# Kernel optimization log

Measured on AMD Instinct MI355X. Metric: run time of the kernel, lower is better.

## Reference

```python
import jax, jax.numpy as jnp
import numpy as np

VOCAB, NUM_TAGS, EMB, HID = 30000, 20, 200, 128
B, S = 128, 512


def setup_inputs() -> dict:
    key = jax.random.key(0)
    ks = jax.random.split(key, 13)
    sentence = jax.random.randint(ks[0], (B, S), 0, VOCAB)
    tags = jax.random.randint(ks[1], (B, S), 0, NUM_TAGS)
    lengths = jax.random.randint(ks[2], (B,), 1, S + 1)
    mask = jnp.arange(S)[None, :] < lengths[:, None]  # [B,S] bool, mask[:,0] all True
    sc = 0.1
    return {
        "sentence": sentence,
        "tags": tags,
        "mask": mask,
        "embedding": jax.random.normal(ks[3], (VOCAB, EMB), jnp.float32) * sc,
        "W_ih": jax.random.normal(ks[4], (4 * HID, EMB), jnp.float32) * sc,
        "W_hh": jax.random.normal(ks[5], (4 * HID, HID), jnp.float32) * sc,
        "b_ih": jax.random.normal(ks[6], (4 * HID,), jnp.float32) * sc,
        "b_hh": jax.random.normal(ks[7], (4 * HID,), jnp.float32) * sc,
        "W_dec": jax.random.normal(ks[8], (NUM_TAGS, HID), jnp.float32) * sc,
        "b_dec": jax.random.normal(ks[9], (NUM_TAGS,), jnp.float32) * sc,
        "start_trans": jax.random.normal(ks[10], (NUM_TAGS,), jnp.float32) * sc,
        "end_trans": jax.random.normal(ks[11], (NUM_TAGS,), jnp.float32) * sc,
        "trans": jax.random.normal(ks[12], (NUM_TAGS, NUM_TAGS), jnp.float32) * sc,
    }


def _lstm(embeds, W_ih, W_hh, b_ih, b_hh):
    # torch nn.LSTM, single layer, batch_first, zero init state; gate order i,f,g,o
    b = embeds.shape[0]
    h0 = jnp.zeros((b, HID), embeds.dtype)
    x = jnp.swapaxes(embeds, 0, 1)  # [S,B,E]
    xg = jnp.einsum('sbe,ge->sbg', x, W_ih) + b_ih + b_hh  # input projections, [S,B,4H]

    def step(carry, xg_t):
        h, c = carry
        g = xg_t + h @ W_hh.T
        i, f, gg, o = jnp.split(g, 4, axis=-1)
        c = jax.nn.sigmoid(f) * c + jax.nn.sigmoid(i) * jnp.tanh(gg)
        h = jax.nn.sigmoid(o) * jnp.tanh(c)
        return (h, c), h

    _, hs = jax.lax.scan(step, (h0, h0), xg)
    return jnp.swapaxes(hs, 0, 1)  # [B,S,H]


def _crf_nll_mean(emissions, tags, mask, start_trans, end_trans, trans):
    # torchcrf.CRF negative log likelihood, reduction='mean' (mean over batch)
    b = emissions.shape[0]
    ems = jnp.swapaxes(emissions, 0, 1)          # [S,B,T]
    tgs = jnp.swapaxes(tags, 0, 1)               # [S,B]
    msk = jnp.swapaxes(mask, 0, 1).astype(emissions.dtype)  # [S,B]
    bidx = jnp.arange(b)

    # numerator: score of the gold path
    num0 = start_trans[tgs[0]] + ems[0, bidx, tgs[0]]

    def nstep(score, inp):
        em, tag, ptag, m = inp
        return score + (trans[ptag, tag] + em[bidx, tag]) * m, None

    num, _ = jax.lax.scan(nstep, num0, (ems[1:], tgs[1:], tgs[:-1], msk[1:]))
    last_idx = mask.sum(axis=1).astype(jnp.int32) - 1
    num = num + end_trans[tags[bidx, last_idx]]

    # denominator: forward algorithm (log partition)
    sc0 = start_trans[None, :] + ems[0]  # [B,T]

    def dstep(score, inp):
        em, m = inp
        nxt = jax.nn.logsumexp(score[:, :, None] + trans[None] + em[:, None, :], axis=1)
        return jnp.where(m[:, None] > 0, nxt, score), None

    sc, _ = jax.lax.scan(dstep, sc0, (ems[1:], msk[1:]))
    den = jax.nn.logsumexp(sc + end_trans[None, :], axis=1)
    return -jnp.mean(num - den)


def reference(sentence, tags, mask, embedding, W_ih, W_hh, b_ih, b_hh,
              W_dec, b_dec, start_trans, end_trans, trans):
    embeds = embedding[sentence]                           # [B,S,E]
    lstm_out = _lstm(embeds, W_ih, W_hh, b_ih, b_hh)       # [B,S,H]
    emissions = jnp.einsum('bsh,th->bst', lstm_out, W_dec) + b_dec  # [B,S,T]
    # dropout treated as identity (eval-mode reference)
    return _crf_nll_mean(emissions, tags, mask, start_trans, end_trans, trans)
```

## Files before the change

### kernel.cpp

```cpp
#include <hip/hip_runtime.h>
#include <hip/hip_bf16.h>
#include <hip/hip_fp16.h>
#include <math.h>

#define B_ 128
#define S_ 512
#define EMB_ 200
#define HID_ 128
#define NT_ 20
#define G4_ 512
#define KP_ 224

typedef _Float16 f16x2_t __attribute__((ext_vector_type(2)));
typedef short bf16x8 __attribute__((ext_vector_type(8)));
typedef float f32x4 __attribute__((ext_vector_type(4)));

#if __has_builtin(__builtin_amdgcn_fdot2)
#define FDOT2(a, b, c) __builtin_amdgcn_fdot2(__builtin_bit_cast(f16x2_t, (a)), \
                                              __builtin_bit_cast(f16x2_t, (b)), (c), false)
#else
static __device__ __forceinline__ float fdot2_fb(unsigned a, unsigned b, float c) {
    float alo = __half2float(__ushort_as_half((unsigned short)(a & 0xffffu)));
    float ahi = __half2float(__ushort_as_half((unsigned short)(a >> 16)));
    float blo = __half2float(__ushort_as_half((unsigned short)(b & 0xffffu)));
    float bhi = __half2float(__ushort_as_half((unsigned short)(b >> 16)));
    return c + alo * blo + ahi * bhi;
}
#define FDOT2(a, b, c) fdot2_fb((a), (b), (c))
#endif

__device__ __forceinline__ float bf2f(unsigned u) {
    union { unsigned u; float f; } cv;
    cv.u = u << 16;
    return cv.f;
}
__device__ __forceinline__ unsigned packh2(float a, float b) {
    return ((unsigned)__half_as_ushort(__float2half(b)) << 16)
         | (unsigned)__half_as_ushort(__float2half(a));
}
__device__ __forceinline__ unsigned short f2bf(float f) {
    __hip_bfloat16 h = __float2bfloat16(f);
    unsigned short u;
    __builtin_memcpy(&u, &h, 2);
    return u;
}

__global__ void k_detect(const unsigned char* mask, int* flag) {
    __shared__ int partial[4];
    int tid = threadIdx.x;
    int s = 0;
    for (int i = tid; i < B_ * S_; i += 256) {
        if (i & 3) s += mask[i];
    }
    for (int m = 32; m >= 1; m >>= 1) s += __shfl_xor(s, m);
    if ((tid & 63) == 0) partial[tid >> 6] = s;
    __syncthreads();
    if (tid == 0) {
        int tot = partial[0] + partial[1] + partial[2] + partial[3];
        flag[0] = (tot > 0) ? 1 : 0;
    }
}

__global__ void k_prep(const float* __restrict__ W_ih, const float* __restrict__ b_ih,
                       const float* __restrict__ b_hh, __hip_bfloat16* __restrict__ Wb,
                       float* __restrict__ biasb) {
    int i = blockIdx.x * 256 + threadIdx.x;
    if (i < G4_ * KP_) {
        int g = i / KP_, k = i - g * KP_;
        float v = (k < EMB_) ? W_ih[g * EMB_ + k] : 0.f;
        Wb[i] = __float2bfloat16(v);
    }
    if (i < G4_) biasb[i] = b_ih[i] + b_hh[i];
}

__global__ __launch_bounds__(256, 2) void k_xg(const int* __restrict__ sentence,
                                               const float* __restrict__ embedding,
                                               const __hip_bfloat16* __restrict__ Wb,
                                               const float* __restrict__ biasb,
                                               __hip_bfloat16* __restrict__ xg) {
    __shared__ short Bl[G4_ * 40];
    __shared__ short Al[32 * 40];
    __shared__ int ids_s[32];
    int tid = threadIdx.x;
    int m0 = blockIdx.x * 32;
    int lane = tid & 63;
    int gbase = (tid >> 6) * 128;
    if (tid < 32) ids_s[tid] = sentence[m0 + tid];
    __syncthreads();

    f32x4 acc0[8], acc1[8];
#pragma unroll
    for (int n = 0; n < 8; n++) {
        acc0[n] = (f32x4){0.f, 0.f, 0.f, 0.f};
        acc1[n] = (f32x4){0.f, 0.f, 0.f, 0.f};
    }
    int lrow = lane & 15, lk = lane >> 4;

    for (int c = 0; c < 7; c++) {
        int k0 = c * 32;
#pragma unroll
        for (int i = 0; i < 8; i++) {
            int idx = tid + 256 * i;
            int row = idx >> 2, q = idx & 3;
            uint4 v = *(const uint4*)((const short*)Wb + (size_t)row * KP_ + k0 + q * 8);
            *(uint4*)(Bl + row * 40 + q * 8) = v;
        }
#pragma unroll
        for (int i = 0; i < 2; i++) {
            int j = tid + 256 * i;
            int row = j >> 4, kp = j & 15;
            int k = k0 + kp * 2;
            const float* e = embedding + (size_t)ids_s[row] * EMB_;
            float v0 = (k < EMB_) ? e[k] : 0.f;
            float v1 = (k + 1 < EMB_) ? e[k + 1] : 0.f;
            unsigned u = (unsigned)f2bf(v0) | ((unsigned)f2bf(v1) << 16);
            *(unsigned*)(Al + row * 40 + kp * 2) = u;
        }
        __syncthreads();
        bf16x8 a0 = *(const bf16x8*)(Al + lrow * 40 + lk * 8);
        bf16x8 a1 = *(const bf16x8*)(Al + (lrow + 16) * 40 + lk * 8);
#pragma unroll
        for (int n = 0; n < 8; n++) {
            bf16x8 bfr = *(const bf16x8*)(Bl + (gbase + n * 16 + lrow) * 40 + lk * 8);
            acc0[n] = __builtin_amdgcn_mfma_f32_16x16x32_bf16(a0, bfr, acc0[n], 0, 0, 0);
            acc1[n] = __builtin_amdgcn_mfma_f32_16x16x32_bf16(a1, bfr, acc1[n], 0, 0, 0);
        }
        __syncthreads();
    }
    int rbase = m0 + lk * 4;
#pragma unroll
    for (int n = 0; n < 8; n++) {
        int g = gbase + n * 16 + lrow;
        float bv = biasb[g];
#pragma unroll
        for (int r = 0; r < 4; r++) {
            xg[(size_t)(rbase + r) * G4_ + g] = __float2bfloat16(acc0[n][r] + bv);
            xg[(size_t)(rbase + r + 16) * G4_ + g] = __float2bfloat16(acc1[n][r] + bv);
        }
    }
}

__global__ __launch_bounds__(1024) __attribute__((amdgpu_waves_per_eu(4, 4)))
void k_lstm(const __hip_bfloat16* __restrict__ xg,
            const float* __restrict__ W_hh,
            unsigned* __restrict__ h2_out) {
    __shared__ unsigned h2_lds[64];
    __shared__ float part_lds[G4_];
    __shared__ float gate_lds[G4_];
    __shared__ ushort xbuf[2][8][G4_];
    int b = blockIdx.x, tid = threadIdx.x;
    int wv = tid >> 6, lane = tid & 63;
    int p = wv >> 3;
    int g = ((wv & 7) << 6) | lane;

    unsigned w2[32];
    const float2* wrow = (const float2*)(W_hh + (size_t)g * HID_ + p * 64);
#pragma unroll
    for (int k = 0; k < 32; k++) {
        float2 f = wrow[k];
        w2[k] = packh2(f.x, f.y);
    }
#pragma unroll
    for (int k = 0; k < 32; k++) asm("" : "+v"(w2[k]));

    const ushort* xgb = (const ushort*)(xg) + (size_t)b * S_ * G4_;
    unsigned* h2b = h2_out + (size_t)b * S_ * 64;

    {
        uint2 v0 = *(const uint2*)(xgb + tid * 4);
        *(uint2*)(&xbuf[0][0][0] + tid * 4) = v0;
    }
    if (tid < 64) h2_lds[tid] = 0u;
    float c0 = 0.f, c1 = 0.f;
    __syncthreads();

    for (int tile = 0; tile < S_ / 8; tile++) {
        int cur = tile & 1;
        int tn = (tile < S_ / 8 - 1) ? tile + 1 : tile;
        uint2 pf = *(const uint2*)(xgb + (size_t)tn * 8 * G4_ + tid * 4);

#pragma unroll
        for (int s = 0; s < 8; s++) {
            int t = tile * 8 + s;
            unsigned xr = 0;
            if (p == 0) xr = xbuf[cur][s][g];
            float a0 = 0.f, a1 = 0.f, a2 = 0.f, a3 = 0.f;
            const uint4* hb4 = (const uint4*)(h2_lds + (p << 5));
#pragma unroll
            for (int q = 0; q < 8; q++) {
                uint4 hh = hb4[q];
                a0 = FDOT2(w2[4 * q + 0], hh.x, a0);
                a1 = FDOT2(w2[4 * q + 1], hh.y, a1);
                a2 = FDOT2(w2[4 * q + 2], hh.z, a2);
                a3 = FDOT2(w2[4 * q + 3], hh.w, a3);
            }
            float acc = (a0 + a1) + (a2 + a3);
            if (p == 1) part_lds[g] = acc;
            __syncthreads();
            if (p == 0) {
                float pre = bf2f(xr) + acc + part_lds[g];
                int gt = g >> 7;
                float xs = (gt == 2) ? 2.f * pre : pre;
                xs = fminf(fmaxf(xs, -30.f), 30.f);
                float r = 1.f / (1.f + __expf(-xs));
                gate_lds[g] = (gt == 2) ? 2.f * r - 1.f : r;
            }
            __syncthreads();
            if (tid < 64) {
                int j = tid;
                float2 iv = *(const float2*)(gate_lds + 2 * j);
                float2 fv = *(const float2*)(gate_lds + 128 + 2 * j);
                float2 gv = *(const float2*)(gate_lds + 256 + 2 * j);
                float2 ov = *(const float2*)(gate_lds + 384 + 2 * j);
                c0 = fv.x * c0 + iv.x * gv.x;
                c1 = fv.y * c1 + iv.y * gv.y;
                float h0 = ov.x * (2.f / (1.f + __expf(-2.f * c0)) - 1.f);
                float h1 = ov.y * (2.f / (1.f + __expf(-2.f * c1)) - 1.f);
                unsigned pk = packh2(h0, h1);
                h2_lds[j] = pk;
                h2b[(size_t)t * 64 + j] = pk;
            }
            __syncthreads();
        }
        *(uint2*)(&xbuf[cur ^ 1][0][0] + tid * 4) = pf;
        __syncthreads();
    }
}

__global__ __launch_bounds__(320) void k_em(const unsigned* __restrict__ h2,
                                            const float* __restrict__ W_dec,
                                            const float* __restrict__ b_dec,
                                            float* __restrict__ em) {
    int half = threadIdx.x / 160;
    int r = threadIdx.x % 160;
    int tag = r >> 3, l8 = r & 7;
    const float* wd = W_dec + tag * HID_ + l8 * 16;
    float ws[16];
#pragma unroll
    for (int q = 0; q < 16; q++) ws[q] = wd[q];
    float bd = b_dec[tag];
    int row0 = blockIdx.x * 16 + half * 8;
    for (int rp = 0; rp < 8; rp++) {
        int row = row0 + rp;
        const uint4* h4 = (const uint4*)(h2 + (size_t)row * 64 + l8 * 8);
        uint4 a = h4[0], bq = h4[1];
        unsigned hv[8] = {a.x, a.y, a.z, a.w, bq.x, bq.y, bq.z, bq.w};
        float pacc = 0.f;
#pragma unroll
        for (int q = 0; q < 8; q++) {
            float lo = __half2float(__ushort_as_half((unsigned short)(hv[q] & 0xffffu)));
            float hi = __half2float(__ushort_as_half((unsigned short)(hv[q] >> 16)));
            pacc += lo * ws[2 * q] + hi * ws[2 * q + 1];
        }
        pacc += __shfl_xor(pacc, 1);
        pacc += __shfl_xor(pacc, 2);
        pacc += __shfl_xor(pacc, 4);
        if (l8 == 0) em[(size_t)row * NT_ + tag] = pacc + bd;
    }
}

__global__ __launch_bounds__(64) void k_crf(const float* __restrict__ em,
                                            const int* __restrict__ tags,
                                            const void* __restrict__ mask,
                                            const int* __restrict__ flag,
                                            const float* __restrict__ start_trans,
                                            const float* __restrict__ end_trans,
                                            const float* __restrict__ trans,
                                            float* __restrict__ nll) {
    __shared__ float em_s[S_ * NT_];
    __shared__ float trans_s[NT_ * NT_];
    __shared__ int tags_s[S_];
    __shared__ unsigned char mask_s[S_];
    __shared__ __align__(16) float score_s[32];
    __shared__ float num_sh;

    int b = blockIdx.x;
    int lane = threadIdx.x;
    const float4* e4 = (const float4*)(em + (size_t)b * S_ * NT_);
    float4* s4 = (float4*)em_s;
    for (int i = lane; i < S_ * NT_ / 4; i += 64) s4[i] = e4[i];
    for (int i = lane; i < NT_ * NT_; i += 64) trans_s[i] = trans[i];
    for (int i = lane; i < S_; i += 64) tags_s[i] = tags[b * S_ + i];
    int fl = flag[0];
    for (int i = lane; i < S_; i += 64) {
        mask_s[i] = fl ? ((const unsigned char*)mask)[b * S_ + i]
                       : (unsigned char)(((const int*)mask)[b * S_ + i] != 0);
    }
    __syncthreads();

    float nsum = 0.f;
    int cnt = 0;
    for (int t = lane; t < S_; t += 64) cnt += mask_s[t];
    for (int t = 1 + lane; t < S_; t += 64) {
        if (mask_s[t]) {
            int tg = tags_s[t], pt = tags_s[t - 1];
            nsum += trans_s[pt * NT_ + tg] + em_s[t * NT_ + tg];
        }
    }
    for (int m = 32; m >= 1; m >>= 1) {
        nsum += __shfl_xor(nsum, m);
        cnt += __shfl_xor(cnt, m);
    }
    if (lane == 0) {
        int t0 = tags_s[0];
        num_sh = nsum + start_trans[t0] + em_s[t0] + end_trans[tags_s[cnt - 1]];
    }

    int tag = (lane < NT_) ? lane : NT_ - 1;
    float tcol[NT_];
#pragma unroll
    for (int p = 0; p < NT_; p++) tcol[p] = trans_s[p * NT_ + tag];
    float sc = start_trans[tag] + em_s[tag];
    if (lane < NT_) score_s[lane] = sc;
    __syncthreads();

    for (int t = 1; t < S_; t++) {
        const float4* q4 = (const float4*)score_s;
        float4 q0 = q4[0], q1 = q4[1], q2 = q4[2], q3 = q4[3], q5 = q4[4];
        float v[NT_] = {q0.x + tcol[0],  q0.y + tcol[1],  q0.z + tcol[2],  q0.w + tcol[3],
                        q1.x + tcol[4],  q1.y + tcol[5],  q1.z + tcol[6],  q1.w + tcol[7],
                        q2.x + tcol[8],  q2.y + tcol[9],  q2.z + tcol[10], q2.w + tcol[11],
                        q3.x + tcol[12], q3.y + tcol[13], q3.z + tcol[14], q3.w + tcol[15],
                        q5.x + tcol[16], q5.y + tcol[17], q5.z + tcol[18], q5.w + tcol[19]};
        float mx[NT_];
#pragma unroll
        for (int p = 0; p < NT_; p++) mx[p] = v[p];
#pragma unroll
        for (int n = NT_; n > 1; n = (n + 1) >> 1) {
#pragma unroll
            for (int i = 0; i < (n >> 1); i++) mx[i] = fmaxf(mx[i], mx[n - 1 - i]);
        }
        float ex[NT_];
#pragma unroll
        for (int p = 0; p < NT_; p++) ex[p] = __expf(v[p] - mx[0]);
#pragma unroll
        for (int n = NT_; n > 1; n = (n + 1) >> 1) {
#pragma unroll
            for (int i = 0; i < (n >> 1); i++) ex[i] += ex[n - 1 - i];
        }
        float nxt = mx[0] + __logf(ex[0]) + em_s[t * NT_ + tag];
        sc = mask_s[t] ? nxt : sc;
        __syncthreads();
        if (lane < NT_) score_s[lane] = sc;
        __syncthreads();
    }

    if (lane < NT_) score_s[lane] = sc + end_trans[tag];
    __syncthreads();
    if (lane == 0) {
        float m = score_s[0];
#pragma unroll
        for (int i = 1; i < NT_; i++) m = fmaxf(m, score_s[i]);
        float s = 0.f;
#pragma unroll
        for (int i = 0; i < NT_; i++) s += __expf(score_s[i] - m);
        nll[b] = (m + __logf(s)) - num_sh;
    }
}

__global__ void k_final(const float* __restrict__ nll, float* __restrict__ out) {
    __shared__ float sums[2];
    int tid = threadIdx.x;
    float v = nll[tid];
    for (int m = 32; m >= 1; m >>= 1) v += __shfl_xor(v, m);
    if ((tid & 63) == 0) sums[tid >> 6] = v;
    __syncthreads();
    if (tid == 0) out[0] = (sums[0] + sums[1]) * (1.f / (float)B_);
}

extern "C" void kernel_launch(void* const* d_in, const int* in_sizes, int n_in,
                              void* d_out, int out_size, void* d_ws, size_t ws_size,
                              hipStream_t stream) {
    const int* sentence = (const int*)d_in[0];
    const int* tags = (const int*)d_in[1];
    const void* mask = d_in[2];
    const float* embedding = (const float*)d_in[3];
    const float* W_ih = (const float*)d_in[4];
    const float* W_hh = (const float*)d_in[5];
    const float* b_ih = (const float*)d_in[6];
    const float* b_hh = (const float*)d_in[7];
    const float* W_dec = (const float*)d_in[8];
    const float* b_dec = (const float*)d_in[9];
    const float* start_trans = (const float*)d_in[10];
    const float* end_trans = (const float*)d_in[11];
    const float* trans = (const float*)d_in[12];

    char* ws = (char*)d_ws;
    int* flag = (int*)ws;
    __hip_bfloat16* xg = (__hip_bfloat16*)(ws + 256);
    size_t off = 256 + (size_t)B_ * S_ * G4_ * 2;
    float* em = (float*)(ws + off);
    off += (size_t)B_ * S_ * NT_ * 4;
    float* nllp = (float*)(ws + off);
    off += 512;
    unsigned* h2_out = (unsigned*)(ws + off);
    off += (size_t)B_ * S_ * 64 * 4;
    __hip_bfloat16* Wb = (__hip_bfloat16*)(ws + off);
    off += (size_t)G4_ * KP_ * 2;
    float* biasb = (float*)(ws + off);

    k_detect<<<1, 256, 0, stream>>>((const unsigned char*)mask, flag);
    k_prep<<<(G4_ * KP_ + 255) / 256, 256, 0, stream>>>(W_ih, b_ih, b_hh, Wb, biasb);
    k_xg<<<(B_ * S_) / 32, 256, 0, stream>>>(sentence, embedding, Wb, biasb, xg);
    k_lstm<<<B_, 1024, 0, stream>>>(xg, W_hh, h2_out);
    k_em<<<(B_ * S_) / 16, 320, 0, stream>>>(h2_out, W_dec, b_dec, em);
    k_crf<<<B_, 64, 0, stream>>>(em, tags, mask, flag, start_trans, end_trans, trans, nllp);
    k_final<<<1, 128, 0, stream>>>(nllp, (float*)d_out);
}
```

Baseline: 726.7 us.

## Restructure LSTM recurrence to one barrier per step using lane shuffles

Reorders the gate columns of the input projection so that each element's four gates sit next to each other, then remaps LSTM threads so that the eight lanes holding one hidden element's four gates (two K-halves each) share a wavefront. The partial dot products and the gate combination now go through cross-lane shuffles instead of LDS, so each timestep needs one barrier instead of three and the block no longer stages input tiles in LDS. Inputs are prefetched two steps ahead straight from global memory, and the hidden state is double-buffered in LDS. In exchange, every thread evaluates its exp redundantly, the sigmoid clamp is dropped, and each step now depends on a per-thread global load latency.

```diff
diff --git a/kernel.cpp b/kernel.cpp
--- a/kernel.cpp
+++ b/kernel.cpp
@@ -28,6 +28,8 @@
 }
 #define FDOT2(a, b, c) fdot2_fb((a), (b), (c))
 #endif
+
+#define BARRIER_LGKM() asm volatile("s_waitcnt lgkmcnt(0)\n\ts_barrier" ::: "memory")
 
 __device__ __forceinline__ float bf2f(unsigned u) {
     union { unsigned u; float f; } cv;
@@ -132,10 +134,11 @@
     for (int n = 0; n < 8; n++) {
         int g = gbase + n * 16 + lrow;
         float bv = biasb[g];
+        int pos = ((g & 127) << 2) | (g >> 7);
 #pragma unroll
         for (int r = 0; r < 4; r++) {
-            xg[(size_t)(rbase + r) * G4_ + g] = __float2bfloat16(acc0[n][r] + bv);
-            xg[(size_t)(rbase + r + 16) * G4_ + g] = __float2bfloat16(acc1[n][r] + bv);
+            xg[(size_t)(rbase + r) * G4_ + pos] = __float2bfloat16(acc0[n][r] + bv);
+            xg[(size_t)(rbase + r + 16) * G4_ + pos] = __float2bfloat16(acc1[n][r] + bv);
         }
     }
 }
@@ -144,17 +147,15 @@
 void k_lstm(const __hip_bfloat16* __restrict__ xg,
             const float* __restrict__ W_hh,
             unsigned* __restrict__ h2_out) {
-    __shared__ unsigned h2_lds[64];
-    __shared__ float part_lds[G4_];
-    __shared__ float gate_lds[G4_];
-    __shared__ ushort xbuf[2][8][G4_];
+    __shared__ ushort hbuf[2][HID_];
     int b = blockIdx.x, tid = threadIdx.x;
     int wv = tid >> 6, lane = tid & 63;
-    int p = wv >> 3;
-    int g = ((wv & 7) << 6) | lane;
+    int el = lane >> 3, gt = (lane >> 1) & 3, half = lane & 1;
+    int e = (wv << 3) | el;
+    int g = (gt << 7) | e;
 
     unsigned w2[32];
-    const float2* wrow = (const float2*)(W_hh + (size_t)g * HID_ + p * 64);
+    const float2* wrow = (const float2*)(W_hh + (size_t)g * HID_ + half * 64);
 #pragma unroll
     for (int k = 0; k < 32; k++) {
         float2 f = wrow[k];
@@ -163,67 +164,49 @@
 #pragma unroll
     for (int k = 0; k < 32; k++) asm("" : "+v"(w2[k]));
 
-    const ushort* xgb = (const ushort*)(xg) + (size_t)b * S_ * G4_;
-    unsigned* h2b = h2_out + (size_t)b * S_ * 64;
-
-    {
-        uint2 v0 = *(const uint2*)(xgb + tid * 4);
-        *(uint2*)(&xbuf[0][0][0] + tid * 4) = v0;
-    }
-    if (tid < 64) h2_lds[tid] = 0u;
-    float c0 = 0.f, c1 = 0.f;
-    __syncthreads();
-
-    for (int tile = 0; tile < S_ / 8; tile++) {
-        int cur = tile & 1;
-        int tn = (tile < S_ / 8 - 1) ? tile + 1 : tile;
-        uint2 pf = *(const uint2*)(xgb + (size_t)tn * 8 * G4_ + tid * 4);
-
-#pragma unroll
-        for (int s = 0; s < 8; s++) {
-            int t = tile * 8 + s;
-            unsigned xr = 0;
-            if (p == 0) xr = xbuf[cur][s][g];
-            float a0 = 0.f, a1 = 0.f, a2 = 0.f, a3 = 0.f;
-            const uint4* hb4 = (const uint4*)(h2_lds + (p << 5));
-#pragma unroll
-            for (int q = 0; q < 8; q++) {
-                uint4 hh = hb4[q];
-                a0 = FDOT2(w2[4 * q + 0], hh.x, a0);
-                a1 = FDOT2(w2[4 * q + 1], hh.y, a1);
-                a2 = FDOT2(w2[4 * q + 2], hh.z, a2);
-                a3 = FDOT2(w2[4 * q + 3], hh.w, a3);
-            }
-            float acc = (a0 + a1) + (a2 + a3);
-            if (p == 1) part_lds[g] = acc;
-            __syncthreads();
-            if (p == 0) {
-                float pre = bf2f(xr) + acc + part_lds[g];
-                int gt = g >> 7;
-                float xs = (gt == 2) ? 2.f * pre : pre;
-                xs = fminf(fmaxf(xs, -30.f), 30.f);
-                float r = 1.f / (1.f + __expf(-xs));
-                gate_lds[g] = (gt == 2) ? 2.f * r - 1.f : r;
-            }
-            __syncthreads();
-            if (tid < 64) {
-                int j = tid;
-                float2 iv = *(const float2*)(gate_lds + 2 * j);
-                float2 fv = *(const float2*)(gate_lds + 128 + 2 * j);
-                float2 gv = *(const float2*)(gate_lds + 256 + 2 * j);
-                float2 ov = *(const float2*)(gate_lds + 384 + 2 * j);
-                c0 = fv.x * c0 + iv.x * gv.x;
-                c1 = fv.y * c1 + iv.y * gv.y;
-                float h0 = ov.x * (2.f / (1.f + __expf(-2.f * c0)) - 1.f);
-                float h1 = ov.y * (2.f / (1.f + __expf(-2.f * c1)) - 1.f);
-                unsigned pk = packh2(h0, h1);
-                h2_lds[j] = pk;
-                h2b[(size_t)t * 64 + j] = pk;
-            }
-            __syncthreads();
-        }
-        *(uint2*)(&xbuf[cur ^ 1][0][0] + tid * 4) = pf;
-        __syncthreads();
+    if (tid < HID_) hbuf[0][tid] = 0;
+    float c = 0.f;
+    const ushort* xp = (const ushort*)(xg) + (size_t)b * S_ * G4_ + (tid >> 1);
+    ushort* hgp = (ushort*)h2_out + (size_t)b * S_ * HID_ + e;
+    bool isg = (gt == 2);
+    bool wLDS = ((lane & 7) == 0);
+    bool wGLB = ((lane & 7) == 1);
+    __syncthreads();
+
+    unsigned xr = xp[0];
+    unsigned xr1 = xp[G4_];
+    for (int t = 0; t < S_; t++) {
+        int t2 = (t + 2 < S_) ? t + 2 : S_ - 1;
+        unsigned xr2 = xp[(size_t)t2 * G4_];
+
+        const uint4* hp = (const uint4*)(hbuf[t & 1]) + (half << 3);
+        float a0 = 0.f, a1 = 0.f, a2 = 0.f, a3 = 0.f;
+#pragma unroll
+        for (int q = 0; q < 8; q++) {
+            uint4 hh = hp[q];
+            a0 = FDOT2(w2[4 * q + 0], hh.x, a0);
+            a1 = FDOT2(w2[4 * q + 1], hh.y, a1);
+            a2 = FDOT2(w2[4 * q + 2], hh.z, a2);
+            a3 = FDOT2(w2[4 * q + 3], hh.w, a3);
+        }
+        float acc = (a0 + a1) + (a2 + a3);
+        acc += __shfl_xor(acc, 1);
+        float pre = bf2f(xr) + acc;
+        float xs = isg ? 2.f * pre : pre;
+        float r = 1.f / (1.f + __expf(-xs));
+        float act = isg ? 2.f * r - 1.f : r;
+
+        float aF = __shfl_xor(act, 2);
+        float aG = __shfl_xor(act, 4);
+        float aO = __shfl_xor(aF, 4);
+        c = aF * c + act * aG;
+        float h = aO * (2.f / (1.f + __expf(-2.f * c)) - 1.f);
+        ushort hu = __half_as_ushort(__float2half(h));
+        if (wLDS) hbuf[(t + 1) & 1][e] = hu;
+        if (wGLB) hgp[(size_t)t * HID_] = hu;
+        BARRIER_LGKM();
+        xr = xr1;
+        xr1 = xr2;
     }
 }
 
```

New measurement: 793.8 us. 9.2% more time.
